# Optimization experiments

Hardware: AMD Instinct MI355X
Metric: run time of the kernel (lower is better)

Reference implementation:

```python
import jax, jax.numpy as jnp
import numpy as np

SW, SH = 240.0, 180.0  # sensor size from LIFSpikePool(..., (240, 180))
EPS = 1e-5


def _grid_edges(gw, gh):
    # static 8-neighbor (king-move) grid graph + self loops, src -> dst
    idx = np.arange(gw * gh).reshape(gh, gw)
    srcs, dsts = [], []
    for dy in (-1, 0, 1):
        for dx in (-1, 0, 1):
            s = idx[max(0, dy):gh - max(0, -dy), max(0, dx):gw - max(0, -dx)]
            d = idx[max(0, -dy):gh - max(0, dy), max(0, -dx):gw - max(0, dx)]
            srcs.append(s.reshape(-1)); dsts.append(d.reshape(-1))
    return (jnp.asarray(np.concatenate(srcs), jnp.int32),
            jnp.asarray(np.concatenate(dsts), jnp.int32))

_E1 = _grid_edges(80, 60)
_E2 = _grid_edges(40, 30)
_E3 = _grid_edges(20, 15)


def _bn(h):
    # BatchNorm1d with gamma=1, beta=0 (per initialize_weights), batch stats
    return (h - h.mean(0)) / jnp.sqrt(h.var(0) + EPS)


def _pnconv(x, pos2, src, dst, W, b):
    # PointNetConv with single-Linear nn: msg = Lin([x_j, pos_j - pos_i]), max-aggr
    n = x.shape[0]
    msg = jnp.concatenate([x[src], pos2[src] - pos2[dst]], axis=1) @ W + b
    agg = jax.ops.segment_max(msg, dst, num_segments=n)
    return jnp.where(jnp.isfinite(agg), agg, 0.0)  # empty segments -> 0


def _block(x, pos, src, dst, c1w, c1b, c2w, c2b, lw, lb):
    p2 = pos[:, :2]
    skip = _bn(x @ lw + lb)
    h = jax.nn.relu(_bn(_pnconv(x, p2, src, dst, c1w, c1b)))
    h = _bn(_pnconv(h, p2, src, dst, c2w, c2b))
    return jax.nn.relu(h + skip)


def _pool(x, pos, gw, gh, W, b):
    # LIF spike pooling: integrate membrane per grid cell, fire if v > 1
    cx = jnp.clip((pos[:, 0] * gw / SW).astype(jnp.int32), 0, gw - 1)
    cy = jnp.clip((pos[:, 1] * gh / SH).astype(jnp.int32), 0, gh - 1)
    cell = cy * gw + cx
    mem = jax.ops.segment_sum(x, cell, num_segments=gw * gh)
    v = mem @ W + b
    xo = jnp.where(v > 1.0, v, 0.0)
    gx, gy = jnp.meshgrid(jnp.arange(gw), jnp.arange(gh))  # (gh, gw)
    npos = jnp.stack([(gx.reshape(-1) + 0.5) * SW / gw,
                      (gy.reshape(-1) + 0.5) * SH / gh,
                      jnp.zeros(gw * gh)], axis=1).astype(jnp.float32)
    return xo, npos


def _forward(edge_index, x, pos, *p):
    src, dst = edge_index[0], edge_index[1]
    h = _block(x, pos, src, dst, *p[0:6])
    h, pos = _pool(h, pos, 80, 60, p[24], p[25])
    h = _block(h, pos, _E1[0], _E1[1], *p[6:12]); feat0 = h   # (4800, 32)
    h, pos = _pool(h, pos, 40, 30, p[26], p[27])
    h = _block(h, pos, _E2[0], _E2[1], *p[12:18]); feat1 = h  # (1200, 64)
    h, pos = _pool(h, pos, 20, 15, p[28], p[29])
    h = _block(h, pos, _E3[0], _E3[1], *p[18:24]); feat2 = h  # (300, 128)
    return feat0, feat1, feat2


PNAMES = [f"b{i}_{t}" for i in (1, 2, 3, 4) for t in ("c1w", "c1b", "c2w", "c2b", "lw", "lb")] + \
         [f"p{j}_{t}" for j in (1, 2, 3) for t in ("w", "b")]


def setup_inputs() -> dict:
    key = jax.random.key(0)
    ks = jax.random.split(key, 20)
    N, E = 200000, 3200000
    x = jax.random.normal(ks[0], (N, 1), jnp.float32)
    pos = jax.random.uniform(ks[1], (N, 3), jnp.float32) * jnp.array([SW, SH, 1.0], jnp.float32)
    edge_index = jax.random.randint(ks[2], (2, E), 0, N, jnp.int32)
    def lin(k, fi, fo):
        return jax.random.normal(k, (fi, fo), jnp.float32) * np.sqrt(2.0 / fi)
    inp = {"x": x, "pos": pos, "edge_index": edge_index}
    ki = 3
    for i, (ci, co) in enumerate([(1, 16), (16, 32), (32, 64), (64, 128)], start=1):
        inp[f"b{i}_c1w"] = lin(ks[ki], ci + 2, co); ki += 1
        inp[f"b{i}_c1b"] = jnp.zeros((co,), jnp.float32)
        inp[f"b{i}_c2w"] = lin(ks[ki], co + 2, co); ki += 1
        inp[f"b{i}_c2b"] = jnp.zeros((co,), jnp.float32)
        inp[f"b{i}_lw"] = lin(ks[ki], ci, co); ki += 1
        inp[f"b{i}_lb"] = jnp.zeros((co,), jnp.float32)
    for j, ch in [(1, 16), (2, 32), (3, 64)]:
        inp[f"p{j}_w"] = lin(ks[ki], ch, ch); ki += 1
        inp[f"p{j}_b"] = jnp.zeros((ch,), jnp.float32)
    return inp


def reference(x, pos, edge_index,
              b1_c1w, b1_c1b, b1_c2w, b1_c2b, b1_lw, b1_lb,
              b2_c1w, b2_c1b, b2_c2w, b2_c2b, b2_lw, b2_lb,
              b3_c1w, b3_c1b, b3_c2w, b3_c2b, b3_lw, b3_lb,
              b4_c1w, b4_c1b, b4_c2w, b4_c2b, b4_lw, b4_lb,
              p1_w, p1_b, p2_w, p2_b, p3_w, p3_b):
    params = (b1_c1w, b1_c1b, b1_c2w, b1_c2b, b1_lw, b1_lb,
              b2_c1w, b2_c1b, b2_c2w, b2_c2b, b2_lw, b2_lb,
              b3_c1w, b3_c1b, b3_c2w, b3_c2b, b3_lw, b3_lb,
              b4_c1w, b4_c1b, b4_c2w, b4_c2b, b4_lw, b4_lb,
              p1_w, p1_b, p2_w, p2_b, p3_w, p3_b)
    return _forward(edge_index, x, pos, *params)
```

## Files before the change

### kernel.cpp

```cpp
#include <hip/hip_runtime.h>

#define NN 200000
#define NE 3200000
#define NWG 80
#define NBKT 196
#define TT 1024
static constexpr float EPSV = 1e-5f;

__device__ __forceinline__ void stwt(float* p, float v){
  __hip_atomic_store(p, v, __ATOMIC_RELAXED, __HIP_MEMORY_SCOPE_AGENT);
}
__device__ __forceinline__ float ldwt(const float* p){
  return __hip_atomic_load(p, __ATOMIC_RELAXED, __HIP_MEMORY_SCOPE_AGENT);
}
__device__ __forceinline__ void stwt_i(int* p, int v){
  __hip_atomic_store(p, v, __ATOMIC_RELAXED, __HIP_MEMORY_SCOPE_AGENT);
}
__device__ __forceinline__ int ldwt_i(const int* p){
  return __hip_atomic_load(p, __ATOMIC_RELAXED, __HIP_MEMORY_SCOPE_AGENT);
}

__device__ __forceinline__ void gridbar(int* bar, int target, int nwg){
  __syncthreads();
  const int t = threadIdx.x;
  if (blockIdx.x == 0){
    if (t >= 1 && t < nwg){
      while (__hip_atomic_load(bar + 32*t, __ATOMIC_RELAXED, __HIP_MEMORY_SCOPE_AGENT) < target)
        __builtin_amdgcn_s_sleep(1);
    }
    __syncthreads();
    if (t == 0)
      __hip_atomic_store(bar + 6272, target, __ATOMIC_RELAXED, __HIP_MEMORY_SCOPE_AGENT);
  } else {
    if (t == 0){
      __atomic_signal_fence(__ATOMIC_SEQ_CST);
      __builtin_amdgcn_s_waitcnt(0);
      __atomic_signal_fence(__ATOMIC_SEQ_CST);
      __hip_atomic_store(bar + 32*blockIdx.x, target, __ATOMIC_RELAXED, __HIP_MEMORY_SCOPE_AGENT);
      while (__hip_atomic_load(bar + 6272, __ATOMIC_RELAXED, __HIP_MEMORY_SCOPE_AGENT) < target)
        __builtin_amdgcn_s_sleep(2);
    }
    __syncthreads();
  }
}

__global__ void k_cnt_prep(const int* __restrict__ ei, int* __restrict__ bktCnt,
                           const float* __restrict__ x, const float* __restrict__ pos,
                           float4* __restrict__ feat, float* __restrict__ xstats){
  __shared__ int cnt[256];
  __shared__ float sv[256], sq[256];
  int t = threadIdx.x;
  cnt[t] = 0;
  int i = blockIdx.x*256 + t;
  float xf = 0.f;
  if (i < NN){
    xf = x[i];
    feat[i] = make_float4(xf, pos[3*i], pos[3*i+1], 0.f);
  }
  sv[t] = (i < NN) ? xf : 0.f;
  sq[t] = sv[t]*sv[t];
  __syncthreads();
  int tile = blockIdx.x*4096;
  #pragma unroll
  for (int k = 0; k < 16; ++k){
    int e = tile + k*256 + t;
    if (e < NE) atomicAdd(&cnt[ei[NE+e]>>10], 1);
  }
  for (int o = 128; o > 0; o >>= 1){
    __syncthreads();
    if (t < o){ sv[t]+=sv[t+o]; sq[t]+=sq[t+o]; }
  }
  __syncthreads();
  if (t == 0){ atomicAdd(&xstats[0], sv[0]); atomicAdd(&xstats[1], sq[0]); }
  if (cnt[t]) atomicAdd(&bktCnt[t], cnt[t]);
}

__device__ __forceinline__ unsigned fenc(float f){
  unsigned u = __float_as_uint(f);
  return (u >> 31) ? ~u : (u | 0x80000000u);
}
__device__ __forceinline__ float fdec(unsigned k){
  unsigned u = (k >> 31) ? (k ^ 0x80000000u) : ~k;
  return __uint_as_float(u);
}
#define ENC_NI 0x007FFFFFu

__global__ void __launch_bounds__(1024) k_b1(const int* __restrict__ ei,
    const int* __restrict__ bktCnt, int* __restrict__ bktBase, int* __restrict__ bktCur,
    int* __restrict__ pairs, const float4* __restrict__ feat, const float* __restrict__ pos,
    const float* __restrict__ w48, const float* __restrict__ biasA,
    const float* __restrict__ w2, float* __restrict__ st1p, float4* __restrict__ A4,
    int* __restrict__ bar){
  __shared__ unsigned acc[16384];
  const int t = threadIdx.x, wg = blockIdx.x;

  if (wg == 0){
    int* s = (int*)acc;
    int v = 0;
    if (t < 256){ v = ldwt_i(&bktCnt[t]); s[t] = v; }
    __syncthreads();
    for (int o = 1; o < 256; o <<= 1){
      int xv = 0;
      if (t >= o && t < 256) xv = s[t-o];
      __syncthreads();
      if (t < 256) s[t] += xv;
      __syncthreads();
    }
    if (t < 256){ stwt_i(&bktBase[t], s[t]-v); stwt_i(&bktCur[t], s[t]-v); }
    if (t == 0) stwt_i(&bktBase[256], NE);
  }
  gridbar(bar, 1, NBKT);

  {
    int* cnt = (int*)acc; int* base = cnt + 256; int* rank = base + 256;
    if (t < 256) cnt[t] = 0;
    __syncthreads();
    int tile = wg*16384;
    #pragma unroll
    for (int k = 0; k < 16; ++k){
      int e = tile + k*1024 + t;
      if (e < NE) atomicAdd(&cnt[ei[NE+e]>>10], 1);
    }
    __syncthreads();
    if (t < 256){
      base[t] = cnt[t] ? atomicAdd(&bktCur[t], cnt[t]) : 0;
      rank[t] = 0;
    }
    __syncthreads();
    #pragma unroll
    for (int k = 0; k < 16; ++k){
      int e = tile + k*1024 + t;
      if (e < NE){
        int d = ei[NE+e], ssrc = ei[e];
        int b = d >> 10;
        int r = atomicAdd(&rank[b], 1);
        stwt_i(&pairs[base[b] + r], (ssrc<<10) | (d & 1023));
      }
    }
  }
  gridbar(bar, 2, NBKT);

  for (int i = t; i < 16384; i += 1024) acc[i] = ENC_NI;
  float wa0[16], wa1[16], wa2[16];
  #pragma unroll
  for (int c = 0; c < 16; ++c){ wa0[c]=w48[c]; wa1[c]=w48[16+c]; wa2[c]=w48[32+c]; }
  const int p0 = ldwt_i(&bktBase[wg]), p1 = ldwt_i(&bktBase[wg+1]);
  __syncthreads();
  for (int j = p0 + t; j < p1; j += 1024){
    int pr = ldwt_i(&pairs[j]);
    float4 f = feat[pr >> 10];
    int d = pr & 1023;
    int gb = d << 4, rot = (d >> 1) & 15;
    #pragma unroll
    for (int c = 0; c < 16; ++c){
      float m = f.x*wa0[c] + f.y*wa1[c] + f.z*wa2[c];
      atomicMax(&acc[gb | ((c + rot) & 15)], fenc(m));
    }
  }
  __syncthreads();
  const int base = wg << 10;
  const int width = min(1024, NN - base);
  {
    const int c = t & 15;
    const float b_c = biasA[c], w1c = w48[16+c], w2c = w48[32+c];
    float ls = 0.f, lq = 0.f;
    for (int i = t; i < width*16; i += 1024){
      int dl = i >> 4, d = base + dl;
      int rot = (dl >> 1) & 15;
      float o = 0.f;
      if (acc[(dl<<4) | rot] != ENC_NI){
        float px = pos[3*d], py = pos[3*d+1];
        o = fdec(acc[(dl<<4) | ((c + rot) & 15)]) + b_c - (px*w1c + py*w2c);
      }
      ls += o; lq += o*o;
    }
    ls += __shfl_xor(ls, 16, 64); ls += __shfl_xor(ls, 32, 64);
    lq += __shfl_xor(lq, 16, 64); lq += __shfl_xor(lq, 32, 64);
    if ((t & 63) < 16){
      int slot = (wg + (t >> 6)) & 15;
      atomicAdd(&st1p[slot*32 + c], ls);
      atomicAdd(&st1p[slot*32 + 16 + c], lq);
    }
  }
  gridbar(bar, 3, NBKT);

  {
    const int lane = t & 63;
    float stv = 0.f;
    if (lane < 32){
      #pragma unroll
      for (int s2 = 0; s2 < 16; ++s2) stv += ldwt(&st1p[s2*32 + lane]);
    }
    const float inv_n = 1.f/(float)NN;
    float mk[16], ik[16];
    #pragma unroll
    for (int k = 0; k < 16; ++k){
      float sm = __shfl(stv, k, 64);
      float sq_ = __shfl(stv, 16 + k, 64);
      float m = sm*inv_n;
      float v = sq_*inv_n - m*m;
      mk[k] = m; ik[k] = rsqrtf(v + EPSV);
    }
    for (int i = t; i < width*4; i += 1024){
      int dl = i >> 2, cg = i & 3, d = base + dl;
      int rot = (dl >> 1) & 15;
      bool valid = (acc[(dl<<4) | rot] != ENC_NI);
      float px = pos[3*d], py = pos[3*d+1];
      float a0=0.f,a1=0.f,a2=0.f,a3=0.f;
      #pragma unroll
      for (int k = 0; k < 16; ++k){
        float o = 0.f;
        if (valid) o = fdec(acc[(dl<<4) | ((k + rot) & 15)]) + biasA[k] - (px*w48[16+k] + py*w48[32+k]);
        float h = fmaxf((o - mk[k])*ik[k], 0.f);
        a0 += h*w2[k*16 + cg*4 + 0];
        a1 += h*w2[k*16 + cg*4 + 1];
        a2 += h*w2[k*16 + cg*4 + 2];
        a3 += h*w2[k*16 + cg*4 + 3];
      }
      int c0 = cg*4;
      a0 += px*w2[256+c0+0] + py*w2[272+c0+0];
      a1 += px*w2[256+c0+1] + py*w2[272+c0+1];
      a2 += px*w2[256+c0+2] + py*w2[272+c0+2];
      a3 += px*w2[256+c0+3] + py*w2[272+c0+3];
      A4[d*4 + cg] = make_float4(a0,a1,a2,a3);
    }
  }
}

__global__ void __launch_bounds__(1024) k_aggBC(const int* __restrict__ pairs, const int* __restrict__ bktBase,
    const float4* __restrict__ A4, const float* __restrict__ pos, const float* __restrict__ x,
    const float* __restrict__ wpos, const float* __restrict__ biasB, const float* __restrict__ lw,
    float* __restrict__ st2p, const float* __restrict__ xstats,
    float* __restrict__ mem1, int* __restrict__ bar){
  __shared__ unsigned acc[16384];
  const int t = threadIdx.x, wg = blockIdx.x;
  for (int i = t; i < 16384; i += 1024) acc[i] = ENC_NI;
  const int p0 = bktBase[wg], p1 = bktBase[wg+1];
  __syncthreads();
  for (int j = p0 + t; j < p1; j += 1024){
    int pr = pairs[j];
    int s = pr >> 10, d = pr & 1023;
    int gb = d << 4, rot = (d >> 1) & 15;
    float4 a0 = A4[s*4+0], a1 = A4[s*4+1], a2 = A4[s*4+2], a3 = A4[s*4+3];
    float av[16] = {a0.x,a0.y,a0.z,a0.w, a1.x,a1.y,a1.z,a1.w,
                    a2.x,a2.y,a2.z,a2.w, a3.x,a3.y,a3.z,a3.w};
    #pragma unroll
    for (int c = 0; c < 16; ++c)
      atomicMax(&acc[gb | ((c + rot) & 15)], fenc(av[c]));
  }
  __syncthreads();
  const int base = wg << 10;
  const int width = min(1024, NN - base);
  const int c = t & 15;
  const float b_c = biasB[c], w1c = wpos[c], w2c = wpos[16+c];
  {
    float ls = 0.f, lq = 0.f;
    for (int i = t; i < width*16; i += 1024){
      int dl = i >> 4, d = base + dl;
      int rot = (dl >> 1) & 15;
      float o = 0.f;
      if (acc[(dl<<4) | rot] != ENC_NI){
        float px = pos[3*d], py = pos[3*d+1];
        o = fdec(acc[(dl<<4) | ((c + rot) & 15)]) + b_c - (px*w1c + py*w2c);
      }
      ls += o; lq += o*o;
    }
    ls += __shfl_xor(ls, 16, 64); ls += __shfl_xor(ls, 32, 64);
    lq += __shfl_xor(lq, 16, 64); lq += __shfl_xor(lq, 32, 64);
    if ((t & 63) < 16){
      int slot = (wg + (t >> 6)) & 15;
      atomicAdd(&st2p[slot*32 + c], ls);
      atomicAdd(&st2p[slot*32 + 16 + c], lq);
    }
  }
  gridbar(bar, 4, NBKT);
  {
    const int lane = t & 63;
    float stv = 0.f;
    if (lane < 32){
      #pragma unroll
      for (int s2 = 0; s2 < 16; ++s2) stv += ldwt(&st2p[s2*32 + lane]);
    }
    const float inv_n = 1.f/(float)NN;
    float sm = __shfl(stv, c, 64), sq_ = __shfl(stv, 16 + c, 64);
    float m2 = sm*inv_n, v2 = sq_*inv_n - m2*m2;
    float i2 = rsqrtf(v2 + EPSV);
    float mx = ldwt(&xstats[0])*inv_n;
    float vx = ldwt(&xstats[1])*inv_n - mx*mx;
    float a = lw[c];
    float sc = a * rsqrtf(a*a*vx + EPSV);
    for (int i = t; i < width*16; i += 1024){
      int dl = i >> 4, d = base + dl;
      int rot = (dl >> 1) & 15;
      float px = pos[3*d], py = pos[3*d+1];
      float o = 0.f;
      if (acc[(dl<<4) | rot] != ENC_NI)
        o = fdec(acc[(dl<<4) | ((c + rot) & 15)]) + b_c - (px*w1c + py*w2c);
      float v = (o - m2)*i2 + (x[d]-mx)*sc;
      v = fmaxf(v, 0.f);
      int cx = (int)(px * 80.f / 240.f); cx = min(max(cx,0),79);
      int cy = (int)(py * 60.f / 180.f); cy = min(max(cy,0),59);
      atomicAdd(&mem1[(cy*80+cx)*16 + c], v);
    }
  }
}

struct TailP {
  const float *mem1;
  const float *p1w,*p1b,*p2w,*p2b,*p3w,*p3b;
  const float *c1w2,*c1b2,*c2w2,*c2b2,*lw2,*lb2;
  const float *c1w3,*c1b3,*c2w3,*c2b3,*lw3,*lb3;
  const float *c1w4,*c1b4,*c2w4,*c2b4,*lw4,*lb4;
  float *g2p,*g3p;
  float *stB2sk,*stB2c1,*stB2c2,*stB3sk,*stB3c1,*stB3c2,*stB4sk,*stB4c1,*stB4c2;
  float *out;
  int *bar;
};

template<int GW,int GH,int TW,int TH,int K,int C,bool FIRST>
__device__ __forceinline__ void ph_A(float* buf, float* sv, float* sq,
    const float* __restrict__ Gglob, const float* __restrict__ plw, const float* __restrict__ plb,
    const float* __restrict__ c1w, const float* __restrict__ c1b,
    const float* __restrict__ lw, const float* __restrict__ lb,
    float* stH1, float* stSK, float sx, float sy, int tile)
{
  constexpr int W2=TW+4, nR2=W2*(TH+4);
  constexpr int W1=TW+2, nR1=W1*(TH+2);
  constexpr int nT=TW*TH, NTX=GW/TW;
  const int tx0=(tile%NTX)*TW, ty0=(tile/NTX)*TH;
  float* Gl=buf; float* Sl=Gl+nR2*K; float* H1l=Sl+nR2*C; float* SKl=H1l+nR1*C;
  const int t=threadIdx.x;
  if constexpr (FIRST){
    for (int e=t; e<nR2*K; e+=TT){
      int cell=e/K, k=e-cell*K;
      int gx=tx0-2+cell%W2, gy=ty0-2+cell/W2;
      Sl[e] = (gx>=0&&gx<GW&&gy>=0&&gy<GH) ? Gglob[(gy*GW+gx)*K+k] : 0.f;
    }
    __syncthreads();
    for (int e=t; e<nR2*K; e+=TT){
      int cell=e/K, c=e-cell*K;
      float acc=plb[c];
      #pragma unroll
      for (int k=0;k<K;++k) acc += Sl[cell*K+k]*plw[k*K+c];
      Gl[e] = (acc>1.f)?acc:0.f;
    }
  } else {
    for (int e=t; e<nR2*K; e+=TT){
      int cell=e/K, k=e-cell*K;
      int gx=tx0-2+cell%W2, gy=ty0-2+cell/W2;
      Gl[e] = (gx>=0&&gx<GW&&gy>=0&&gy<GH) ? ldwt(&Gglob[(gy*GW+gx)*K+k]) : 0.f;
    }
  }
  __syncthreads();
  for (int e=t; e<nR2*C; e+=TT){
    int cell=e/C, c=e-cell*C;
    float acc=0.f;
    #pragma unroll 8
    for (int k=0;k<K;++k) acc += Gl[cell*K+k]*c1w[k*C+c];
    Sl[e]=acc;
  }
  float ls=0.f,lq=0.f;
  for (int e=t; e<nT*C; e+=TT){
    int cell=e/C, c=e-cell*C;
    int lx=cell%TW, ly=cell/TW;
    int g2=(ly+2)*W2+(lx+2);
    float acc=lb[c];
    #pragma unroll 8
    for (int k=0;k<K;++k) acc += Gl[g2*K+k]*lw[k*C+c];
    SKl[e]=acc; ls+=acc; lq+=acc*acc;
  }
  __syncthreads();
  sv[t]=ls; sq[t]=lq; __syncthreads();
  for (int o=TT/2;o>=C;o>>=1){ if(t<o){sv[t]+=sv[t+o];sq[t]+=sq[t+o];} __syncthreads(); }
  if (t<C){ atomicAdd(&stSK[t],sv[t]); atomicAdd(&stSK[C+t],sq[t]); }
  __syncthreads();
  ls=0.f; lq=0.f;
  const float NI=-__builtin_inff();
  for (int e=t; e<nR1*C; e+=TT){
    int cell=e/C, c=e-cell*C;
    int lx=cell%W1, ly=cell/W1;
    int gx=tx0-1+lx, gy=ty0-1+ly;
    if (gx<0||gx>=GW||gy<0||gy>=GH) continue;
    float wx=c1w[K*C+c], wy=c1w[(K+1)*C+c];
    float m=NI;
    #pragma unroll
    for (int oy=-1;oy<=1;++oy){
      int ny=gy+oy; if (ny<0||ny>=GH) continue;
      #pragma unroll
      for (int ox=-1;ox<=1;++ox){
        int nx=gx+ox; if (nx<0||nx>=GW) continue;
        int l2=(ly+1+oy)*W2+(lx+1+ox);
        m=fmaxf(m, Sl[l2*C+c]+(ox*sx)*wx+(oy*sy)*wy);
      }
    }
    float val=m+c1b[c];
    H1l[e]=val;
    if (gx>=tx0&&gx<tx0+TW&&gy>=ty0&&gy<ty0+TH){ ls+=val; lq+=val*val; }
  }
  __syncthreads();
  sv[t]=ls; sq[t]=lq; __syncthreads();
  for (int o=TT/2;o>=C;o>>=1){ if(t<o){sv[t]+=sv[t+o];sq[t]+=sq[t+o];} __syncthreads(); }
  if (t<C){ atomicAdd(&stH1[t],sv[t]); atomicAdd(&stH1[C+t],sq[t]); }
}

template<int GW,int GH,int TW,int TH,int K,int C>
__device__ __forceinline__ void ph_B(float* buf, float* sv, float* sq, float* la, float* lbv,
    const float* __restrict__ c2w, const float* __restrict__ c2b,
    const float* stH1, float* stH2, float sx, float sy, int tile)
{
  constexpr int W2=TW+4, nR2=W2*(TH+4);
  constexpr int W1=TW+2, nR1=W1*(TH+2);
  constexpr int nT=TW*TH, NTX=GW/TW;
  const int tx0=(tile%NTX)*TW, ty0=(tile/NTX)*TH;
  float* Gl=buf; float* Sl=Gl+nR2*K; float* H1l=Sl+nR2*C; float* SKl=H1l+nR1*C; float* H2l=SKl+nT*C;
  const int t=threadIdx.x;
  const float invn=1.f/(float)(GW*GH);
  if (t<C){
    float mk=ldwt(&stH1[t])*invn;
    float vk=ldwt(&stH1[C+t])*invn - mk*mk;
    float ik=rsqrtf(vk+EPSV);
    la[t]=ik; lbv[t]=-mk*ik;
  }
  __syncthreads();
  for (int e=t;e<nR1*C;e+=TT){
    int cell=e/C,c=e-cell*C;
    int gx=tx0-1+cell%W1, gy=ty0-1+cell/W1;
    if (gx<0||gx>=GW||gy<0||gy>=GH) continue;
    H1l[e]=fmaxf(H1l[e]*la[c]+lbv[c],0.f);
  }
  __syncthreads();
  for (int e=t;e<nR1*C;e+=TT){
    int cell=e/C,c=e-cell*C;
    int gx=tx0-1+cell%W1, gy=ty0-1+cell/W1;
    if (gx<0||gx>=GW||gy<0||gy>=GH) continue;
    float acc=0.f;
    #pragma unroll 8
    for (int k=0;k<C;++k) acc += H1l[cell*C+k]*c2w[k*C+c];
    Sl[e]=acc;
  }
  __syncthreads();
  float ls=0.f,lq=0.f;
  const float NI=-__builtin_inff();
  for (int e=t;e<nT*C;e+=TT){
    int cell=e/C,c=e-cell*C;
    int lx=cell%TW, ly=cell/TW;
    int gx=tx0+lx, gy=ty0+ly;
    float wx=c2w[C*C+c], wy=c2w[(C+1)*C+c];
    float m=NI;
    #pragma unroll
    for (int oy=-1;oy<=1;++oy){
      int ny=gy+oy; if (ny<0||ny>=GH) continue;
      #pragma unroll
      for (int ox=-1;ox<=1;++ox){
        int nx=gx+ox; if (nx<0||nx>=GW) continue;
        int l1=(ly+1+oy)*W1+(lx+1+ox);
        m=fmaxf(m, Sl[l1*C+c]+(ox*sx)*wx+(oy*sy)*wy);
      }
    }
    float val=m+c2b[c];
    H2l[e]=val; ls+=val; lq+=val*val;
  }
  __syncthreads();
  sv[t]=ls; sq[t]=lq; __syncthreads();
  for (int o=TT/2;o>=C;o>>=1){ if(t<o){sv[t]+=sv[t+o];sq[t]+=sq[t+o];} __syncthreads(); }
  if (t<C){ atomicAdd(&stH2[t],sv[t]); atomicAdd(&stH2[C+t],sq[t]); }
}

template<int GW,int GH,int TW,int TH,int K,int C,bool POOL>
__device__ __forceinline__ void ph_C(float* buf, float* asv, float* asq, float* la, float* lbv,
    const float* stH2, const float* stSK,
    const float* __restrict__ pw, const float* __restrict__ pb,
    float* __restrict__ outg, float* __restrict__ Gpg, int tile)
{
  constexpr int W2=TW+4, nR2=W2*(TH+4);
  constexpr int W1=TW+2, nR1=W1*(TH+2);
  constexpr int nT=TW*TH, NTX=GW/TW;
  const int tx0=(tile%NTX)*TW, ty0=(tile/NTX)*TH;
  float* Gl=buf; float* Sl=Gl+nR2*K; float* H1l=Sl+nR2*C; float* SKl=H1l+nR1*C; float* H2l=SKl+nT*C;
  const int t=threadIdx.x;
  const float invn=1.f/(float)(GW*GH);
  if (t<C){
    float m2=ldwt(&stH2[t])*invn, v2=ldwt(&stH2[C+t])*invn-m2*m2;
    float i2=rsqrtf(v2+EPSV);
    la[t]=i2; lbv[t]=-m2*i2;
    float ms=ldwt(&stSK[t])*invn, vs=ldwt(&stSK[C+t])*invn-ms*ms;
    float is_=rsqrtf(vs+EPSV);
    asv[t]=is_; asq[t]=-ms*is_;
  }
  __syncthreads();
  float* OUTl=Sl;
  for (int e=t;e<nT*C;e+=TT){
    int cell=e/C,c=e-cell*C;
    int lx=cell%TW, ly=cell/TW;
    int gx=tx0+lx, gy=ty0+ly;
    float v=(H2l[e]*la[c]+lbv[c])+(SKl[e]*asv[c]+asq[c]);
    v=fmaxf(v,0.f);
    outg[(gy*GW+gx)*C+c]=v;
    OUTl[e]=v;
  }
  if constexpr (POOL){
    __syncthreads();
    constexpr int PTW=TW/2, PTH=TH/2, nP=PTW*PTH, PGW=GW/2;
    float* Ml=H1l;
    for (int e=t;e<nP*C;e+=TT){
      int pc=e/C,c=e-pc*C;
      int plx=pc%PTW, ply=pc/PTW;
      float s=0.f;
      #pragma unroll
      for (int dy=0;dy<2;++dy)
        #pragma unroll
        for (int dx=0;dx<2;++dx)
          s += OUTl[((2*ply+dy)*TW+(2*plx+dx))*C+c];
      Ml[e]=s;
    }
    __syncthreads();
    for (int e=t;e<nP*C;e+=TT){
      int pc=e/C,c=e-pc*C;
      int plx=pc%PTW, ply=pc/PTW;
      float acc=pb[c];
      #pragma unroll 8
      for (int k=0;k<C;++k) acc += Ml[pc*C+k]*pw[k*C+c];
      int gpx=tx0/2+plx, gpy=ty0/2+ply;
      stwt(&Gpg[(gpy*PGW+gpx)*C+c], (acc>1.f)?acc:0.f);
    }
  }
  (void)nR1;
}

__global__ void __launch_bounds__(TT) k_tail(TailP P){
  __shared__ float sv[TT], sq[TT], la[128], lbv[128];
  __shared__ float buf[13824];
  int* bar = P.bar;
  const int tile = blockIdx.x;

  if (tile < 80) ph_A<80,60,10,6,16,32,true >(buf,sv,sq,P.mem1,P.p1w,P.p1b,P.c1w2,P.c1b2,P.lw2,P.lb2,P.stB2c1,P.stB2sk,3.f,3.f,tile);
  gridbar(bar, 5, NWG);
  if (tile < 80) ph_B<80,60,10,6,16,32>(buf,sv,sq,la,lbv,P.c2w2,P.c2b2,P.stB2c1,P.stB2c2,3.f,3.f,tile);
  gridbar(bar, 6, NWG);
  if (tile < 80) ph_C<80,60,10,6,16,32,true >(buf,sv,sq,la,lbv,P.stB2c2,P.stB2sk,P.p2w,P.p2b,P.out,P.g2p,tile);
  gridbar(bar, 7, NWG);
  if (tile < 50) ph_A<40,30,4,6,32,64,false>(buf,sv,sq,P.g2p,nullptr,nullptr,P.c1w3,P.c1b3,P.lw3,P.lb3,P.stB3c1,P.stB3sk,6.f,6.f,tile);
  gridbar(bar, 8, NWG);
  if (tile < 50) ph_B<40,30,4,6,32,64>(buf,sv,sq,la,lbv,P.c2w3,P.c2b3,P.stB3c1,P.stB3c2,6.f,6.f,tile);
  gridbar(bar, 9, NWG);
  if (tile < 50) ph_C<40,30,4,6,32,64,true >(buf,sv,sq,la,lbv,P.stB3c2,P.stB3sk,P.p3w,P.p3b,P.out+153600,P.g3p,tile);
  gridbar(bar, 10, NWG);
  if (tile < 50) ph_A<20,15,2,3,64,128,false>(buf,sv,sq,P.g3p,nullptr,nullptr,P.c1w4,P.c1b4,P.lw4,P.lb4,P.stB4c1,P.stB4sk,12.f,12.f,tile);
  gridbar(bar, 11, NWG);
  if (tile < 50) ph_B<20,15,2,3,64,128>(buf,sv,sq,la,lbv,P.c2w4,P.c2b4,P.stB4c1,P.stB4c2,12.f,12.f,tile);
  gridbar(bar, 12, NWG);
  if (tile < 50) ph_C<20,15,2,3,64,128,false>(buf,sv,sq,la,lbv,P.stB4c2,P.stB4sk,nullptr,nullptr,P.out+230400,nullptr,tile);
}

extern "C" void kernel_launch(void* const* d_in, const int* in_sizes, int n_in,
                              void* d_out, int out_size, void* d_ws, size_t ws_size,
                              hipStream_t stream){
  const float* x   = (const float*)d_in[0];
  const float* pos = (const float*)d_in[1];
  const int*   ei  = (const int*)d_in[2];
  const float* b1_c1w = (const float*)d_in[3];
  const float* b1_c1b = (const float*)d_in[4];
  const float* b1_c2w = (const float*)d_in[5];
  const float* b1_c2b = (const float*)d_in[6];
  const float* b1_lw  = (const float*)d_in[7];
  const float* b2_c1w = (const float*)d_in[9];
  const float* b2_c1b = (const float*)d_in[10];
  const float* b2_c2w = (const float*)d_in[11];
  const float* b2_c2b = (const float*)d_in[12];
  const float* b2_lw  = (const float*)d_in[13];
  const float* b2_lb  = (const float*)d_in[14];
  const float* b3_c1w = (const float*)d_in[15];
  const float* b3_c1b = (const float*)d_in[16];
  const float* b3_c2w = (const float*)d_in[17];
  const float* b3_c2b = (const float*)d_in[18];
  const float* b3_lw  = (const float*)d_in[19];
  const float* b3_lb  = (const float*)d_in[20];
  const float* b4_c1w = (const float*)d_in[21];
  const float* b4_c1b = (const float*)d_in[22];
  const float* b4_c2w = (const float*)d_in[23];
  const float* b4_c2b = (const float*)d_in[24];
  const float* b4_lw  = (const float*)d_in[25];
  const float* b4_lb  = (const float*)d_in[26];
  const float* p1w = (const float*)d_in[27];
  const float* p1b = (const float*)d_in[28];
  const float* p2w = (const float*)d_in[29];
  const float* p2b = (const float*)d_in[30];
  const float* p3w = (const float*)d_in[31];
  const float* p3b = (const float*)d_in[32];
  float* out = (float*)d_out;

  float4* feat = (float4*)d_ws;
  float* A  = (float*)(feat + NN);
  float* g2p  = A;
  float* g3p  = A + 38400;
  int* bktCnt  = (int*)(A + NN*16);
  int* bktBase = bktCnt + 256;
  int* bktCur  = bktBase + 257;
  int* bar     = bktCnt + 1024;
  float* STz   = (float*)(bktCnt + 1024 + 6400);
  float* xstats = STz;
  float* st1p   = STz + 64;
  float* st2p   = STz + 576;
  float* stB2sk = STz + 1088;
  float* stB2c1 = STz + 1152;
  float* stB2c2 = STz + 1216;
  float* stB3sk = STz + 1280;
  float* stB3c1 = STz + 1408;
  float* stB3c2 = STz + 1536;
  float* stB4sk = STz + 1664;
  float* stB4c1 = STz + 1920;
  float* stB4c2 = STz + 2176;
  float* mem1   = STz + 2560;
  const size_t ZBYTES = (size_t)(1024 + 6400 + 2560 + 76800) * 4;
  int* pairs  = (int*)(mem1 + 76800);

  hipMemsetAsync(bktCnt, 0, ZBYTES, stream);

  k_cnt_prep<<<(NE+4095)/4096, 256, 0, stream>>>(ei, bktCnt, x, pos, feat, xstats);
  k_b1   <<<NBKT, TT, 0, stream>>>(ei, bktCnt, bktBase, bktCur, pairs, feat, pos,
                                   b1_c1w, b1_c1b, b1_c2w, st1p, (float4*)A, bar);
  k_aggBC<<<NBKT, TT, 0, stream>>>(pairs, bktBase, (const float4*)A, pos, x,
                                   b1_c2w+256, b1_c2b, b1_lw, st2p, xstats, mem1, bar);

  TailP P;
  P.mem1 = mem1;
  P.p1w = p1w; P.p1b = p1b; P.p2w = p2w; P.p2b = p2b; P.p3w = p3w; P.p3b = p3b;
  P.c1w2 = b2_c1w; P.c1b2 = b2_c1b; P.c2w2 = b2_c2w; P.c2b2 = b2_c2b; P.lw2 = b2_lw; P.lb2 = b2_lb;
  P.c1w3 = b3_c1w; P.c1b3 = b3_c1b; P.c2w3 = b3_c2w; P.c2b3 = b3_c2b; P.lw3 = b3_lw; P.lb3 = b3_lb;
  P.c1w4 = b4_c1w; P.c1b4 = b4_c1b; P.c2w4 = b4_c2w; P.c2b4 = b4_c2b; P.lw4 = b4_lw; P.lb4 = b4_lb;
  P.g2p = g2p; P.g3p = g3p;
  P.stB2sk = stB2sk; P.stB2c1 = stB2c1; P.stB2c2 = stB2c2;
  P.stB3sk = stB3sk; P.stB3c1 = stB3c1; P.stB3c2 = stB3c2;
  P.stB4sk = stB4sk; P.stB4c1 = stB4c1; P.stB4c2 = stB4c2;
  P.out = out; P.bar = bar;
  k_tail<<<NWG, TT, 0, stream>>>(P);
}
```

Before: 447.9 us.

## Split bucket scan and edge partition out of fused persistent kernel into separate launches

The bucket prefix scan and the edge-to-bucket partition, which ran inside the persistent k_b1 kernel behind two software grid barriers, now run as two standalone kernels (a one-block scan and a partition kernel). Kernel boundaries replace the grid barriers, so plain loads and stores take the place of the agent-scope atomic loads and stores. Barrier target numbers are renumbered to match. This removes spin-wait barrier overhead and atomic-store traffic but adds two kernel launches and their launch gaps.

```diff
diff --git a/kernel.cpp b/kernel.cpp
--- a/kernel.cpp
+++ b/kernel.cpp
@@ -11,12 +11,6 @@
   __hip_atomic_store(p, v, __ATOMIC_RELAXED, __HIP_MEMORY_SCOPE_AGENT);
 }
 __device__ __forceinline__ float ldwt(const float* p){
-  return __hip_atomic_load(p, __ATOMIC_RELAXED, __HIP_MEMORY_SCOPE_AGENT);
-}
-__device__ __forceinline__ void stwt_i(int* p, int v){
-  __hip_atomic_store(p, v, __ATOMIC_RELAXED, __HIP_MEMORY_SCOPE_AGENT);
-}
-__device__ __forceinline__ int ldwt_i(const int* p){
   return __hip_atomic_load(p, __ATOMIC_RELAXED, __HIP_MEMORY_SCOPE_AGENT);
 }
 
@@ -75,6 +69,52 @@
   if (cnt[t]) atomicAdd(&bktCnt[t], cnt[t]);
 }
 
+__global__ void k_bktscan(const int* __restrict__ bktCnt, int* __restrict__ bktBase,
+                          int* __restrict__ bktCur){
+  __shared__ int s[256];
+  int t = threadIdx.x;
+  int v = bktCnt[t];
+  s[t] = v; __syncthreads();
+  for (int o = 1; o < 256; o <<= 1){
+    int xv = (t >= o) ? s[t-o] : 0;
+    __syncthreads(); s[t] += xv; __syncthreads();
+  }
+  int excl = s[t] - v;
+  bktBase[t] = excl;
+  bktCur[t]  = excl;
+  if (t == 0){ bktBase[256] = NE; }
+}
+
+__global__ void k_part1(const int* __restrict__ ei, int* __restrict__ bktCur,
+                        int* __restrict__ pairs){
+  __shared__ int cnt[256]; __shared__ int base[256]; __shared__ int rank[256];
+  int t = threadIdx.x;
+  if (t < 256) cnt[t] = 0;
+  __syncthreads();
+  int tile = blockIdx.x*16384;
+  #pragma unroll
+  for (int k = 0; k < 16; ++k){
+    int e = tile + k*1024 + t;
+    if (e < NE) atomicAdd(&cnt[ei[NE+e]>>10], 1);
+  }
+  __syncthreads();
+  if (t < 256){
+    base[t] = cnt[t] ? atomicAdd(&bktCur[t], cnt[t]) : 0;
+    rank[t] = 0;
+  }
+  __syncthreads();
+  #pragma unroll
+  for (int k = 0; k < 16; ++k){
+    int e = tile + k*1024 + t;
+    if (e < NE){
+      int d = ei[NE+e], s = ei[e];
+      int b = d >> 10;
+      int r = atomicAdd(&rank[b], 1);
+      pairs[base[b] + r] = (s<<10) | (d & 1023);
+    }
+  }
+}
+
 __device__ __forceinline__ unsigned fenc(float f){
   unsigned u = __float_as_uint(f);
   return (u >> 31) ? ~u : (u | 0x80000000u);
@@ -85,69 +125,21 @@
 }
 #define ENC_NI 0x007FFFFFu
 
-__global__ void __launch_bounds__(1024) k_b1(const int* __restrict__ ei,
-    const int* __restrict__ bktCnt, int* __restrict__ bktBase, int* __restrict__ bktCur,
-    int* __restrict__ pairs, const float4* __restrict__ feat, const float* __restrict__ pos,
+__global__ void __launch_bounds__(1024) k_b1f(const int* __restrict__ pairs, const int* __restrict__ bktBase,
+    const float4* __restrict__ feat, const float* __restrict__ pos,
     const float* __restrict__ w48, const float* __restrict__ biasA,
     const float* __restrict__ w2, float* __restrict__ st1p, float4* __restrict__ A4,
     int* __restrict__ bar){
   __shared__ unsigned acc[16384];
   const int t = threadIdx.x, wg = blockIdx.x;
-
-  if (wg == 0){
-    int* s = (int*)acc;
-    int v = 0;
-    if (t < 256){ v = ldwt_i(&bktCnt[t]); s[t] = v; }
-    __syncthreads();
-    for (int o = 1; o < 256; o <<= 1){
-      int xv = 0;
-      if (t >= o && t < 256) xv = s[t-o];
-      __syncthreads();
-      if (t < 256) s[t] += xv;
-      __syncthreads();
-    }
-    if (t < 256){ stwt_i(&bktBase[t], s[t]-v); stwt_i(&bktCur[t], s[t]-v); }
-    if (t == 0) stwt_i(&bktBase[256], NE);
-  }
-  gridbar(bar, 1, NBKT);
-
-  {
-    int* cnt = (int*)acc; int* base = cnt + 256; int* rank = base + 256;
-    if (t < 256) cnt[t] = 0;
-    __syncthreads();
-    int tile = wg*16384;
-    #pragma unroll
-    for (int k = 0; k < 16; ++k){
-      int e = tile + k*1024 + t;
-      if (e < NE) atomicAdd(&cnt[ei[NE+e]>>10], 1);
-    }
-    __syncthreads();
-    if (t < 256){
-      base[t] = cnt[t] ? atomicAdd(&bktCur[t], cnt[t]) : 0;
-      rank[t] = 0;
-    }
-    __syncthreads();
-    #pragma unroll
-    for (int k = 0; k < 16; ++k){
-      int e = tile + k*1024 + t;
-      if (e < NE){
-        int d = ei[NE+e], ssrc = ei[e];
-        int b = d >> 10;
-        int r = atomicAdd(&rank[b], 1);
-        stwt_i(&pairs[base[b] + r], (ssrc<<10) | (d & 1023));
-      }
-    }
-  }
-  gridbar(bar, 2, NBKT);
-
   for (int i = t; i < 16384; i += 1024) acc[i] = ENC_NI;
   float wa0[16], wa1[16], wa2[16];
   #pragma unroll
   for (int c = 0; c < 16; ++c){ wa0[c]=w48[c]; wa1[c]=w48[16+c]; wa2[c]=w48[32+c]; }
-  const int p0 = ldwt_i(&bktBase[wg]), p1 = ldwt_i(&bktBase[wg+1]);
+  const int p0 = bktBase[wg], p1 = bktBase[wg+1];
   __syncthreads();
   for (int j = p0 + t; j < p1; j += 1024){
-    int pr = ldwt_i(&pairs[j]);
+    int pr = pairs[j];
     float4 f = feat[pr >> 10];
     int d = pr & 1023;
     int gb = d << 4, rot = (d >> 1) & 15;
@@ -182,8 +174,7 @@
       atomicAdd(&st1p[slot*32 + 16 + c], lq);
     }
   }
-  gridbar(bar, 3, NBKT);
-
+  gridbar(bar, 1, NBKT);
   {
     const int lane = t & 63;
     float stv = 0.f;
@@ -227,7 +218,7 @@
   }
 }
 
-__global__ void __launch_bounds__(1024) k_aggBC(const int* __restrict__ pairs, const int* __restrict__ bktBase,
+__global__ void __launch_bounds__(1024) k_b2f(const int* __restrict__ pairs, const int* __restrict__ bktBase,
     const float4* __restrict__ A4, const float* __restrict__ pos, const float* __restrict__ x,
     const float* __restrict__ wpos, const float* __restrict__ biasB, const float* __restrict__ lw,
     float* __restrict__ st2p, const float* __restrict__ xstats,
@@ -273,7 +264,7 @@
       atomicAdd(&st2p[slot*32 + 16 + c], lq);
     }
   }
-  gridbar(bar, 4, NBKT);
+  gridbar(bar, 2, NBKT);
   {
     const int lane = t & 63;
     float stv = 0.f;
@@ -534,21 +525,21 @@
   const int tile = blockIdx.x;
 
   if (tile < 80) ph_A<80,60,10,6,16,32,true >(buf,sv,sq,P.mem1,P.p1w,P.p1b,P.c1w2,P.c1b2,P.lw2,P.lb2,P.stB2c1,P.stB2sk,3.f,3.f,tile);
+  gridbar(bar, 3, NWG);
+  if (tile < 80) ph_B<80,60,10,6,16,32>(buf,sv,sq,la,lbv,P.c2w2,P.c2b2,P.stB2c1,P.stB2c2,3.f,3.f,tile);
+  gridbar(bar, 4, NWG);
+  if (tile < 80) ph_C<80,60,10,6,16,32,true >(buf,sv,sq,la,lbv,P.stB2c2,P.stB2sk,P.p2w,P.p2b,P.out,P.g2p,tile);
   gridbar(bar, 5, NWG);
-  if (tile < 80) ph_B<80,60,10,6,16,32>(buf,sv,sq,la,lbv,P.c2w2,P.c2b2,P.stB2c1,P.stB2c2,3.f,3.f,tile);
+  if (tile < 50) ph_A<40,30,4,6,32,64,false>(buf,sv,sq,P.g2p,nullptr,nullptr,P.c1w3,P.c1b3,P.lw3,P.lb3,P.stB3c1,P.stB3sk,6.f,6.f,tile);
   gridbar(bar, 6, NWG);
-  if (tile < 80) ph_C<80,60,10,6,16,32,true >(buf,sv,sq,la,lbv,P.stB2c2,P.stB2sk,P.p2w,P.p2b,P.out,P.g2p,tile);
+  if (tile < 50) ph_B<40,30,4,6,32,64>(buf,sv,sq,la,lbv,P.c2w3,P.c2b3,P.stB3c1,P.stB3c2,6.f,6.f,tile);
   gridbar(bar, 7, NWG);
-  if (tile < 50) ph_A<40,30,4,6,32,64,false>(buf,sv,sq,P.g2p,nullptr,nullptr,P.c1w3,P.c1b3,P.lw3,P.lb3,P.stB3c1,P.stB3sk,6.f,6.f,tile);
+  if (tile < 50) ph_C<40,30,4,6,32,64,true >(buf,sv,sq,la,lbv,P.stB3c2,P.stB3sk,P.p3w,P.p3b,P.out+153600,P.g3p,tile);
   gridbar(bar, 8, NWG);
-  if (tile < 50) ph_B<40,30,4,6,32,64>(buf,sv,sq,la,lbv,P.c2w3,P.c2b3,P.stB3c1,P.stB3c2,6.f,6.f,tile);
+  if (tile < 50) ph_A<20,15,2,3,64,128,false>(buf,sv,sq,P.g3p,nullptr,nullptr,P.c1w4,P.c1b4,P.lw4,P.lb4,P.stB4c1,P.stB4sk,12.f,12.f,tile);
   gridbar(bar, 9, NWG);
-  if (tile < 50) ph_C<40,30,4,6,32,64,true >(buf,sv,sq,la,lbv,P.stB3c2,P.stB3sk,P.p3w,P.p3b,P.out+153600,P.g3p,tile);
+  if (tile < 50) ph_B<20,15,2,3,64,128>(buf,sv,sq,la,lbv,P.c2w4,P.c2b4,P.stB4c1,P.stB4c2,12.f,12.f,tile);
   gridbar(bar, 10, NWG);
-  if (tile < 50) ph_A<20,15,2,3,64,128,false>(buf,sv,sq,P.g3p,nullptr,nullptr,P.c1w4,P.c1b4,P.lw4,P.lb4,P.stB4c1,P.stB4sk,12.f,12.f,tile);
-  gridbar(bar, 11, NWG);
-  if (tile < 50) ph_B<20,15,2,3,64,128>(buf,sv,sq,la,lbv,P.c2w4,P.c2b4,P.stB4c1,P.stB4c2,12.f,12.f,tile);
-  gridbar(bar, 12, NWG);
   if (tile < 50) ph_C<20,15,2,3,64,128,false>(buf,sv,sq,la,lbv,P.stB4c2,P.stB4sk,nullptr,nullptr,P.out+230400,nullptr,tile);
 }
 
@@ -617,9 +608,11 @@
   hipMemsetAsync(bktCnt, 0, ZBYTES, stream);
 
   k_cnt_prep<<<(NE+4095)/4096, 256, 0, stream>>>(ei, bktCnt, x, pos, feat, xstats);
-  k_b1   <<<NBKT, TT, 0, stream>>>(ei, bktCnt, bktBase, bktCur, pairs, feat, pos,
+  k_bktscan <<<1, 256, 0, stream>>>(bktCnt, bktBase, bktCur);
+  k_part1   <<<(NE+16383)/16384, 1024, 0, stream>>>(ei, bktCur, pairs);
+  k_b1f  <<<NBKT, TT, 0, stream>>>(pairs, bktBase, feat, pos,
                                    b1_c1w, b1_c1b, b1_c2w, st1p, (float4*)A, bar);
-  k_aggBC<<<NBKT, TT, 0, stream>>>(pairs, bktBase, (const float4*)A, pos, x,
+  k_b2f  <<<NBKT, TT, 0, stream>>>(pairs, bktBase, (const float4*)A, pos, x,
                                    b1_c2w+256, b1_c2b, b1_lw, st2p, xstats, mem1, bar);
 
   TailP P;
```

New measurement: 428.3 us. -4.4%, faster.

## Store conv2 pre-activations in fp16 and fuse edge bucketing into one kernel

Applied to the files above, without the earlier changes.

The per-node second-conv linear output is now written as packed half-precision values. The position term of that linear is no longer baked in at the source node; it is recomputed per edge from the source features, so the per-edge gather reads half as many bytes. The edge counting, prefix scan and scatter into destination buckets move out of the first conv kernel into a new build kernel that synchronises with grid barriers. That kernel now writes the pairs with plain stores instead of atomic stores. Storing in fp16 adds rounding error to the max aggregation and later batch-norm statistics.

```diff
diff --git a/kernel.cpp b/kernel.cpp
--- a/kernel.cpp
+++ b/kernel.cpp
@@ -1,4 +1,5 @@
 #include <hip/hip_runtime.h>
+#include <hip/hip_fp16.h>
 
 #define NN 200000
 #define NE 3200000
@@ -44,14 +45,17 @@
   }
 }
 
-__global__ void k_cnt_prep(const int* __restrict__ ei, int* __restrict__ bktCnt,
-                           const float* __restrict__ x, const float* __restrict__ pos,
-                           float4* __restrict__ feat, float* __restrict__ xstats){
-  __shared__ int cnt[256];
-  __shared__ float sv[256], sq[256];
-  int t = threadIdx.x;
-  cnt[t] = 0;
-  int i = blockIdx.x*256 + t;
+__global__ void __launch_bounds__(1024) k_build(const int* __restrict__ ei,
+    const float* __restrict__ x, const float* __restrict__ pos,
+    float4* __restrict__ feat, float* __restrict__ xstats,
+    int* __restrict__ bktCnt, int* __restrict__ bktBase, int* __restrict__ bktCur,
+    int* __restrict__ pairs, int* __restrict__ bar){
+  __shared__ int cnt[256]; __shared__ int base[256]; __shared__ int rank[256];
+  __shared__ float sv[1024], sq[1024];
+  const int t = threadIdx.x, wg = blockIdx.x;
+  const int tile = wg*16384;
+  if (t < 256) cnt[t] = 0;
+  int i = wg*1024 + t;
   float xf = 0.f;
   if (i < NN){
     xf = x[i];
@@ -60,19 +64,49 @@
   sv[t] = (i < NN) ? xf : 0.f;
   sq[t] = sv[t]*sv[t];
   __syncthreads();
-  int tile = blockIdx.x*4096;
   #pragma unroll
   for (int k = 0; k < 16; ++k){
-    int e = tile + k*256 + t;
+    int e = tile + k*1024 + t;
     if (e < NE) atomicAdd(&cnt[ei[NE+e]>>10], 1);
   }
-  for (int o = 128; o > 0; o >>= 1){
+  for (int o = 512; o > 0; o >>= 1){
     __syncthreads();
     if (t < o){ sv[t]+=sv[t+o]; sq[t]+=sq[t+o]; }
   }
   __syncthreads();
   if (t == 0){ atomicAdd(&xstats[0], sv[0]); atomicAdd(&xstats[1], sq[0]); }
-  if (cnt[t]) atomicAdd(&bktCnt[t], cnt[t]);
+  if (t < 256 && cnt[t]) atomicAdd(&bktCnt[t], cnt[t]);
+  gridbar(bar, 1, NBKT);
+  if (wg == 0){
+    int v = 0;
+    if (t < 256){ v = ldwt_i(&bktCnt[t]); base[t] = v; }
+    __syncthreads();
+    for (int o = 1; o < 256; o <<= 1){
+      int xv = 0;
+      if (t >= o && t < 256) xv = base[t-o];
+      __syncthreads();
+      if (t < 256) base[t] += xv;
+      __syncthreads();
+    }
+    if (t < 256){ stwt_i(&bktBase[t], base[t]-v); stwt_i(&bktCur[t], base[t]-v); }
+    if (t == 0) stwt_i(&bktBase[256], NE);
+  }
+  gridbar(bar, 2, NBKT);
+  if (t < 256){
+    base[t] = cnt[t] ? atomicAdd(&bktCur[t], cnt[t]) : 0;
+    rank[t] = 0;
+  }
+  __syncthreads();
+  #pragma unroll
+  for (int k = 0; k < 16; ++k){
+    int e = tile + k*1024 + t;
+    if (e < NE){
+      int d = ei[NE+e], s = ei[e];
+      int b = d >> 10;
+      int r = atomicAdd(&rank[b], 1);
+      pairs[base[b] + r] = (s<<10) | (d & 1023);
+    }
+  }
 }
 
 __device__ __forceinline__ unsigned fenc(float f){
@@ -85,69 +119,21 @@
 }
 #define ENC_NI 0x007FFFFFu
 
-__global__ void __launch_bounds__(1024) k_b1(const int* __restrict__ ei,
-    const int* __restrict__ bktCnt, int* __restrict__ bktBase, int* __restrict__ bktCur,
-    int* __restrict__ pairs, const float4* __restrict__ feat, const float* __restrict__ pos,
+__global__ void __launch_bounds__(1024) k_b1f(const int* __restrict__ pairs, const int* __restrict__ bktBase,
+    const float4* __restrict__ feat, const float* __restrict__ pos,
     const float* __restrict__ w48, const float* __restrict__ biasA,
-    const float* __restrict__ w2, float* __restrict__ st1p, float4* __restrict__ A4,
+    const float* __restrict__ w2, float* __restrict__ st1p, uint2* __restrict__ A2,
     int* __restrict__ bar){
   __shared__ unsigned acc[16384];
   const int t = threadIdx.x, wg = blockIdx.x;
-
-  if (wg == 0){
-    int* s = (int*)acc;
-    int v = 0;
-    if (t < 256){ v = ldwt_i(&bktCnt[t]); s[t] = v; }
-    __syncthreads();
-    for (int o = 1; o < 256; o <<= 1){
-      int xv = 0;
-      if (t >= o && t < 256) xv = s[t-o];
-      __syncthreads();
-      if (t < 256) s[t] += xv;
-      __syncthreads();
-    }
-    if (t < 256){ stwt_i(&bktBase[t], s[t]-v); stwt_i(&bktCur[t], s[t]-v); }
-    if (t == 0) stwt_i(&bktBase[256], NE);
-  }
-  gridbar(bar, 1, NBKT);
-
-  {
-    int* cnt = (int*)acc; int* base = cnt + 256; int* rank = base + 256;
-    if (t < 256) cnt[t] = 0;
-    __syncthreads();
-    int tile = wg*16384;
-    #pragma unroll
-    for (int k = 0; k < 16; ++k){
-      int e = tile + k*1024 + t;
-      if (e < NE) atomicAdd(&cnt[ei[NE+e]>>10], 1);
-    }
-    __syncthreads();
-    if (t < 256){
-      base[t] = cnt[t] ? atomicAdd(&bktCur[t], cnt[t]) : 0;
-      rank[t] = 0;
-    }
-    __syncthreads();
-    #pragma unroll
-    for (int k = 0; k < 16; ++k){
-      int e = tile + k*1024 + t;
-      if (e < NE){
-        int d = ei[NE+e], ssrc = ei[e];
-        int b = d >> 10;
-        int r = atomicAdd(&rank[b], 1);
-        stwt_i(&pairs[base[b] + r], (ssrc<<10) | (d & 1023));
-      }
-    }
-  }
-  gridbar(bar, 2, NBKT);
-
   for (int i = t; i < 16384; i += 1024) acc[i] = ENC_NI;
   float wa0[16], wa1[16], wa2[16];
   #pragma unroll
   for (int c = 0; c < 16; ++c){ wa0[c]=w48[c]; wa1[c]=w48[16+c]; wa2[c]=w48[32+c]; }
-  const int p0 = ldwt_i(&bktBase[wg]), p1 = ldwt_i(&bktBase[wg+1]);
+  const int p0 = bktBase[wg], p1 = bktBase[wg+1];
   __syncthreads();
   for (int j = p0 + t; j < p1; j += 1024){
-    int pr = ldwt_i(&pairs[j]);
+    int pr = pairs[j];
     float4 f = feat[pr >> 10];
     int d = pr & 1023;
     int gb = d << 4, rot = (d >> 1) & 15;
@@ -183,7 +169,6 @@
     }
   }
   gridbar(bar, 3, NBKT);
-
   {
     const int lane = t & 63;
     float stv = 0.f;
@@ -217,36 +202,53 @@
         a2 += h*w2[k*16 + cg*4 + 2];
         a3 += h*w2[k*16 + cg*4 + 3];
       }
-      int c0 = cg*4;
-      a0 += px*w2[256+c0+0] + py*w2[272+c0+0];
-      a1 += px*w2[256+c0+1] + py*w2[272+c0+1];
-      a2 += px*w2[256+c0+2] + py*w2[272+c0+2];
-      a3 += px*w2[256+c0+3] + py*w2[272+c0+3];
-      A4[d*4 + cg] = make_float4(a0,a1,a2,a3);
-    }
-  }
-}
-
-__global__ void __launch_bounds__(1024) k_aggBC(const int* __restrict__ pairs, const int* __restrict__ bktBase,
-    const float4* __restrict__ A4, const float* __restrict__ pos, const float* __restrict__ x,
+      __half2 h01 = __floats2half2_rn(a0, a1);
+      __half2 h23 = __floats2half2_rn(a2, a3);
+      uint2 pk;
+      pk.x = *reinterpret_cast<unsigned*>(&h01);
+      pk.y = *reinterpret_cast<unsigned*>(&h23);
+      A2[d*4 + cg] = pk;
+    }
+  }
+}
+
+__global__ void __launch_bounds__(1024) k_b2f(const int* __restrict__ pairs, const int* __restrict__ bktBase,
+    const uint4* __restrict__ Ah, const float4* __restrict__ feat,
+    const float* __restrict__ pos, const float* __restrict__ x,
     const float* __restrict__ wpos, const float* __restrict__ biasB, const float* __restrict__ lw,
     float* __restrict__ st2p, const float* __restrict__ xstats,
     float* __restrict__ mem1, int* __restrict__ bar){
   __shared__ unsigned acc[16384];
   const int t = threadIdx.x, wg = blockIdx.x;
   for (int i = t; i < 16384; i += 1024) acc[i] = ENC_NI;
+  float wx[16], wy[16];
+  #pragma unroll
+  for (int c = 0; c < 16; ++c){ wx[c]=wpos[c]; wy[c]=wpos[16+c]; }
   const int p0 = bktBase[wg], p1 = bktBase[wg+1];
   __syncthreads();
   for (int j = p0 + t; j < p1; j += 1024){
     int pr = pairs[j];
     int s = pr >> 10, d = pr & 1023;
     int gb = d << 4, rot = (d >> 1) & 15;
-    float4 a0 = A4[s*4+0], a1 = A4[s*4+1], a2 = A4[s*4+2], a3 = A4[s*4+3];
-    float av[16] = {a0.x,a0.y,a0.z,a0.w, a1.x,a1.y,a1.z,a1.w,
-                    a2.x,a2.y,a2.z,a2.w, a3.x,a3.y,a3.z,a3.w};
+    float4 f = feat[s];
+    uint4 q0 = Ah[s*2+0], q1 = Ah[s*2+1];
+    float m[16];
+    {
+      float2 u;
+      u = __half22float2(*reinterpret_cast<__half2*>(&q0.x)); m[0]=u.x;  m[1]=u.y;
+      u = __half22float2(*reinterpret_cast<__half2*>(&q0.y)); m[2]=u.x;  m[3]=u.y;
+      u = __half22float2(*reinterpret_cast<__half2*>(&q0.z)); m[4]=u.x;  m[5]=u.y;
+      u = __half22float2(*reinterpret_cast<__half2*>(&q0.w)); m[6]=u.x;  m[7]=u.y;
+      u = __half22float2(*reinterpret_cast<__half2*>(&q1.x)); m[8]=u.x;  m[9]=u.y;
+      u = __half22float2(*reinterpret_cast<__half2*>(&q1.y)); m[10]=u.x; m[11]=u.y;
+      u = __half22float2(*reinterpret_cast<__half2*>(&q1.z)); m[12]=u.x; m[13]=u.y;
+      u = __half22float2(*reinterpret_cast<__half2*>(&q1.w)); m[14]=u.x; m[15]=u.y;
+    }
     #pragma unroll
-    for (int c = 0; c < 16; ++c)
-      atomicMax(&acc[gb | ((c + rot) & 15)], fenc(av[c]));
+    for (int c = 0; c < 16; ++c){
+      float mv = m[c] + f.y*wx[c] + f.z*wy[c];
+      atomicMax(&acc[gb | ((c + rot) & 15)], fenc(mv));
+    }
   }
   __syncthreads();
   const int base = wg << 10;
@@ -616,10 +618,10 @@
 
   hipMemsetAsync(bktCnt, 0, ZBYTES, stream);
 
-  k_cnt_prep<<<(NE+4095)/4096, 256, 0, stream>>>(ei, bktCnt, x, pos, feat, xstats);
-  k_b1   <<<NBKT, TT, 0, stream>>>(ei, bktCnt, bktBase, bktCur, pairs, feat, pos,
-                                   b1_c1w, b1_c1b, b1_c2w, st1p, (float4*)A, bar);
-  k_aggBC<<<NBKT, TT, 0, stream>>>(pairs, bktBase, (const float4*)A, pos, x,
+  k_build<<<NBKT, TT, 0, stream>>>(ei, x, pos, feat, xstats, bktCnt, bktBase, bktCur, pairs, bar);
+  k_b1f  <<<NBKT, TT, 0, stream>>>(pairs, bktBase, feat, pos,
+                                   b1_c1w, b1_c1b, b1_c2w, st1p, (uint2*)A, bar);
+  k_b2f  <<<NBKT, TT, 0, stream>>>(pairs, bktBase, (const uint4*)A, feat, pos, x,
                                    b1_c2w+256, b1_c2b, b1_lw, st2p, xstats, mem1, bar);
 
   TailP P;
```

Result: faster. 409.9 us (-8.5%).
